# Kernel tuning notes

Hardware: AMD Instinct MI355X
Metric: run time of the kernel (lower is better)

The kernel has to match this reference:

```python
import jax, jax.numpy as jnp
import numpy as np

V, E, H, L, C = 50257, 256, 256, 2, 64
B, T = 4, 48
MASK_ID = 103
EPS = 1e-5
SAMPLE_KEY = jax.random.key(1234)


def lstm_cell(x, h, c, Wih, Whh, bih, bhh):
    # PyTorch gate order: i, f, g, o
    z = x @ Wih.T + h @ Whh.T + (bih + bhh)  # [B,4H]
    i, f, g, o = jnp.split(z, 4, axis=-1)
    c = jax.nn.sigmoid(f) * c + jax.nn.sigmoid(i) * jnp.tanh(g)
    h = jax.nn.sigmoid(o) * jnp.tanh(c)
    return h, c


def setup_inputs() -> dict:
    key = jax.random.key(0)
    ks = jax.random.split(key, 16)
    g = lambda k, s: (jax.random.normal(k, s, dtype=jnp.float32) * 0.05)
    emb = g(ks[0], (V, E)).at[0].set(0.0)  # padding_idx=0 row zeroed
    params = dict(
        emb=emb,
        W_e2e=g(ks[1], (H, E)), b_e2e=jnp.zeros((H,), jnp.float32),
        W_e2d=g(ks[2], (H, E)), b_e2d=jnp.zeros((H,), jnp.float32),
        enc_Wih=g(ks[3], (L, 4 * H, H)), enc_Whh=g(ks[4], (L, 4 * H, H)),
        enc_bih=jnp.zeros((L, 4 * H), jnp.float32), enc_bhh=jnp.zeros((L, 4 * H), jnp.float32),
        dec_Wih=g(ks[5], (L, 4 * H, H)), dec_Whh=g(ks[6], (L, 4 * H, H)),
        dec_bih=jnp.zeros((L, 4 * H), jnp.float32), dec_bhh=jnp.zeros((L, 4 * H), jnp.float32),
        W_cls=g(ks[7], (C, 1)), b_cls=jnp.zeros((C,), jnp.float32),
        W_fc1=g(ks[8], (H + C, H + C)), b_fc1=jnp.zeros((H + C,), jnp.float32),
        ln_g=jnp.ones((H + C,), jnp.float32), ln_b=jnp.zeros((H + C,), jnp.float32),
        W_fc2=g(ks[9], (V, H + C)), b_fc2=jnp.zeros((V,), jnp.float32),
    )
    input_ids = jax.random.randint(ks[10], (B, T), 0, V, dtype=jnp.int32)
    mask_pos = jax.random.bernoulli(ks[11], 0.3, (B, T))  # ensure masked slots exist
    input_ids = jnp.where(mask_pos, jnp.int32(MASK_ID), input_ids)
    attention_mask = jnp.ones((B, T), jnp.int32)
    classification_labels = jax.random.bernoulli(ks[12], 0.5, (B,)).astype(jnp.float32)
    return dict(input_ids=input_ids, attention_mask=attention_mask,
                classification_labels=classification_labels, **params)


def _forward(input_ids, classification_labels, emb, W_e2e, b_e2e, W_e2d, b_e2d,
             enc_Wih, enc_Whh, enc_bih, enc_bhh, dec_Wih, dec_Whh, dec_bih, dec_bhh,
             W_cls, b_cls, W_fc1, b_fc1, ln_g, ln_b, W_fc2, b_fc2):
    f32 = jnp.float32
    # ---- encoder: embed -> linear+relu (dropout=eval identity) -> 2-layer LSTM ----
    xe = jax.nn.relu(emb[input_ids] @ W_e2e.T + b_e2e)  # [B,T,H]
    xs = jnp.swapaxes(xe, 0, 1)  # [T,B,H]
    h0 = jnp.zeros((L, B, H), f32)

    def enc_step(hc, xj):
        h, c = hc
        cur, hs, cs = xj, [], []
        for l in range(L):
            nh, nc = lstm_cell(cur, h[l], c[l], enc_Wih[l], enc_Whh[l], enc_bih[l], enc_bhh[l])
            hs.append(nh); cs.append(nc); cur = nh
        return (jnp.stack(hs), jnp.stack(cs)), None

    (h, c), _ = jax.lax.scan(enc_step, (h0, h0), xs)

    # classifier states are loop-invariant in the original (hoisted, same math)
    cls_states = classification_labels[:, None] @ W_cls.T + b_cls  # [B,C]

    tokens0 = jnp.zeros((B, T), input_ids.dtype).at[:, 0].set(input_ids[:, 0])

    def decode_step(carry, t):
        tokens, h, c = carry
        # re-embed the ENTIRE current prefix, as the original does each step
        x = jax.nn.relu(emb[tokens] @ W_e2d.T + b_e2d)  # [B,T,H]
        xs_t = jnp.swapaxes(x, 0, 1)  # [T,B,H]

        def mstep(hc, inp):
            hh, cc = hc
            xj, j = inp
            cur, hs, cs = xj, [], []
            for l in range(L):
                nh, nc = lstm_cell(cur, hh[l], cc[l], dec_Wih[l], dec_Whh[l], dec_bih[l], dec_bhh[l])
                hs.append(nh); cs.append(nc); cur = nh
            nh, nc = jnp.stack(hs), jnp.stack(cs)
            valid = j < t  # only positions 0..t-1 are real prefix tokens
            hh = jnp.where(valid, nh, hh)
            cc = jnp.where(valid, nc, cc)
            return (hh, cc), hh[-1]

        (h, c), ys = jax.lax.scan(mstep, (h, c), (xs_t, jnp.arange(T)))
        dec_out = jax.lax.dynamic_index_in_dim(ys, t - 1, axis=0, keepdims=False)  # [B,H]

        z = jnp.concatenate([dec_out, cls_states], axis=-1)  # [B,H+C]
        z1 = jax.nn.relu(z @ W_fc1.T + b_fc1)
        mu = z1.mean(-1, keepdims=True)
        var = ((z1 - mu) ** 2).mean(-1, keepdims=True)
        z1 = (z1 - mu) * jax.lax.rsqrt(var + EPS) * ln_g + ln_b
        logits = z1 @ W_fc2.T + b_fc2  # [B,V]
        logp = jax.nn.log_softmax(logits, axis=-1)

        gumb = jax.random.gumbel(jax.random.fold_in(SAMPLE_KEY, t), logp.shape)
        sampled = jnp.argmax(logp + gumb, axis=-1)  # [B] categorical sample
        slp = jnp.take_along_axis(logp, sampled[:, None], axis=-1)[:, 0]  # [B]

        cur_tok = jnp.take(input_ids, t, axis=1)  # [B]
        next_tok = jnp.where(cur_tok == MASK_ID, sampled.astype(tokens.dtype), cur_tok)
        tokens = jax.lax.dynamic_update_slice(tokens, next_tok[:, None], (0, t))
        return (tokens, h, c), slp

    (tokens, h, c), slps = jax.lax.scan(decode_step, (tokens0, h, c), jnp.arange(1, T))
    scores = jnp.concatenate([jnp.zeros((B, 1), f32), slps.T], axis=1)  # [B,T]
    return scores, tokens


def reference(input_ids, attention_mask, classification_labels, emb, W_e2e, b_e2e,
              W_e2d, b_e2d, enc_Wih, enc_Whh, enc_bih, enc_bhh, dec_Wih, dec_Whh,
              dec_bih, dec_bhh, W_cls, b_cls, W_fc1, b_fc1, ln_g, ln_b, W_fc2, b_fc2):
    # attention_mask is accepted but unused, matching the original forward
    return _forward(input_ids, classification_labels, emb, W_e2e, b_e2e, W_e2d, b_e2d,
                    enc_Wih, enc_Whh, enc_bih, enc_bhh, dec_Wih, dec_Whh, dec_bih, dec_bhh,
                    W_cls, b_cls, W_fc1, b_fc1, ln_g, ln_b, W_fc2, b_fc2)
```

## Files before the change

kernel.cpp:

```cpp
#include <hip/hip_runtime.h>
#include <stdint.h>
#include <stddef.h>
#include <math.h>


#define PARTITIONABLE_PRNG 1

namespace s2sr {

constexpr int kV = 50257, kE = 256, kH = 256, kCc = 64, kB = 4, kT = 48;
constexpr int kZ = kH + kCc;
constexpr int kG = 4 * kH;
constexpr int kMask = 103;
constexpr float kEps = 1e-5f;
constexpr float kTiny = 1.17549435e-38f;

constexpr int NWG = 256, TPB = 256;
constexpr int NCL = 32;
constexpr int LEAD = 32;
constexpr int GANG0 = 33;
constexpr int NGANG = NWG - GANG0;
constexpr int RPW = (kV + NGANG - 1) / NGANG;
constexpr int NPX = 16;

constexpr int SH_H0 = 0;
constexpr int SH_H1 = 1024;
constexpr int SH_P0 = 2048;
constexpr int SH_P1 = 3072;
constexpr int SH_Z  = 4096;
constexpr int SH_TOT = 4608;
constexpr int LD_ZIN = 0;
constexpr int LD_Z1  = 1280;
constexpr int LD_CLS = 2560;
constexpr int LD_LSE = 2816;
constexpr int LD_WPS = 2820;

struct alignas(128) Tag { unsigned v; unsigned _p[31]; };
struct alignas(128) GOut {
  unsigned long long key[kB];
  float ps[kB];
  unsigned tag;
  unsigned _p[19];
};

struct SyncBlk {
  Tag ictr, igen;
  Tag ctag[NCL];
  Tag ptok[NPX];
  Tag hzT;
  Tag zT;
  Tag eT;
  GOut gout[NGANG];
};

struct WS {
  SyncBlk s;
  float h0buf[2][kB][kH];
  float h1buf[2][kB][kH];
  float hz[2][kB][kH];
  float z1n[2][kB][kZ];
  float xcur[kB][kH];
  float xd0[kB][kH];
  float px0[kT][kB][kG];
  float pxe[kT][kB][kG];
};

__device__ __forceinline__ float aldf(const float* p) {
  return __hip_atomic_load(p, __ATOMIC_RELAXED, __HIP_MEMORY_SCOPE_AGENT);
}
__device__ __forceinline__ void astf(float* p, float v) {
  __hip_atomic_store(p, v, __ATOMIC_RELAXED, __HIP_MEMORY_SCOPE_AGENT);
}
__device__ __forceinline__ unsigned ldu(const unsigned* p) {
  return __hip_atomic_load(p, __ATOMIC_RELAXED, __HIP_MEMORY_SCOPE_AGENT);
}
__device__ __forceinline__ void relTag(Tag* tg, unsigned v) {
  __hip_atomic_store(&tg->v, v, __ATOMIC_RELEASE, __HIP_MEMORY_SCOPE_AGENT);
}
template <int SLP>
__device__ __forceinline__ void spinTag(Tag* tg, unsigned tgt) {
  if (threadIdx.x == 0) {
    while (ldu(&tg->v) < tgt) __builtin_amdgcn_s_sleep(SLP);
    __atomic_signal_fence(__ATOMIC_ACQUIRE);
  }
  __syncthreads();
}
__device__ __forceinline__ void cbar(SyncBlk* sb, unsigned& ep, int cw) {
  __syncthreads();
  ep += 1u;
  const int tid = (int)threadIdx.x;
  if (tid == 0) relTag(&sb->ctag[cw], ep);
  if (tid < NCL) {
    while (ldu(&sb->ctag[tid].v) < ep) {}
    __atomic_signal_fence(__ATOMIC_ACQUIRE);
  }
  __syncthreads();
}
__device__ __forceinline__ void wait_ptok(SyncBlk* sb, unsigned tgt) {
  if (threadIdx.x < NPX) {
    while (ldu(&sb->ptok[threadIdx.x].v) < tgt) {}
    __atomic_signal_fence(__ATOMIC_ACQUIRE);
  }
  __syncthreads();
}
__device__ __forceinline__ void gbar(SyncBlk* sb, unsigned tgt) {
  __syncthreads();
  if (threadIdx.x == 0) {
    const unsigned old = __hip_atomic_fetch_add(&sb->ictr.v, 1u, __ATOMIC_RELEASE,
                                                __HIP_MEMORY_SCOPE_AGENT);
    if (old == tgt - 1u) relTag(&sb->igen, tgt);
    while (ldu(&sb->igen.v) < tgt) __builtin_amdgcn_s_sleep(2);
    __atomic_signal_fence(__ATOMIC_ACQUIRE);
  }
  __syncthreads();
}

__device__ __forceinline__ unsigned rotl32(unsigned v, int n) {
  return (v << n) | (v >> (32 - n));
}
__device__ __forceinline__ void tf2x32(unsigned k0, unsigned k1, unsigned x0, unsigned x1,
                                       unsigned& o0, unsigned& o1) {
  const unsigned k2 = k0 ^ k1 ^ 0x1BD11BDAu;
  unsigned v0 = x0 + k0, v1 = x1 + k1;
  v0 += v1; v1 = rotl32(v1, 13); v1 ^= v0;
  v0 += v1; v1 = rotl32(v1, 15); v1 ^= v0;
  v0 += v1; v1 = rotl32(v1, 26); v1 ^= v0;
  v0 += v1; v1 = rotl32(v1, 6);  v1 ^= v0;
  v0 += k1; v1 += k2 + 1u;
  v0 += v1; v1 = rotl32(v1, 17); v1 ^= v0;
  v0 += v1; v1 = rotl32(v1, 29); v1 ^= v0;
  v0 += v1; v1 = rotl32(v1, 16); v1 ^= v0;
  v0 += v1; v1 = rotl32(v1, 24); v1 ^= v0;
  v0 += k2; v1 += k0 + 2u;
  v0 += v1; v1 = rotl32(v1, 13); v1 ^= v0;
  v0 += v1; v1 = rotl32(v1, 15); v1 ^= v0;
  v0 += v1; v1 = rotl32(v1, 26); v1 ^= v0;
  v0 += v1; v1 = rotl32(v1, 6);  v1 ^= v0;
  v0 += k0; v1 += k1 + 3u;
  v0 += v1; v1 = rotl32(v1, 17); v1 ^= v0;
  v0 += v1; v1 = rotl32(v1, 29); v1 ^= v0;
  v0 += v1; v1 = rotl32(v1, 16); v1 ^= v0;
  v0 += v1; v1 = rotl32(v1, 24); v1 ^= v0;
  v0 += k1; v1 += k2 + 4u;
  v0 += v1; v1 = rotl32(v1, 13); v1 ^= v0;
  v0 += v1; v1 = rotl32(v1, 15); v1 ^= v0;
  v0 += v1; v1 = rotl32(v1, 26); v1 ^= v0;
  v0 += v1; v1 = rotl32(v1, 6);  v1 ^= v0;
  o0 = v0 + k2; o1 = v1 + k0 + 5u;
}
__device__ __forceinline__ unsigned rbits(unsigned k0, unsigned k1, unsigned i) {
#if PARTITIONABLE_PRNG
  unsigned a, b; tf2x32(k0, k1, 0u, i, a, b);
  return a ^ b;
#else
  constexpr unsigned HALF = (unsigned)((kB * kV + 1) / 2);
  unsigned a, b;
  if (i < HALF) { tf2x32(k0, k1, i, i + HALF, a, b); return a; }
  tf2x32(k0, k1, i - HALF, i, a, b); return b;
#endif
}
__device__ __forceinline__ float gumbel_from_bits(unsigned bits) {
  float f = __uint_as_float((bits >> 9) | 0x3f800000u) - 1.0f;
  f = fmaxf(f, kTiny);
  return -logf(-logf(f));
}
__device__ __forceinline__ unsigned ordkey(float f) {
  const unsigned u = __float_as_uint(f);
  return (u & 0x80000000u) ? ~u : (u | 0x80000000u);
}
__device__ __forceinline__ unsigned long long shflx64(unsigned long long v, int m) {
  unsigned lo = (unsigned)v, hi = (unsigned)(v >> 32);
  lo = (unsigned)__shfl_xor((int)lo, m, 64);
  hi = (unsigned)__shfl_xor((int)hi, m, 64);
  return ((unsigned long long)hi << 32) | (unsigned long long)lo;
}
__device__ __forceinline__ float sigm(float x) { return 1.0f / (1.0f + expf(-x)); }

template <bool STREAM>
__device__ __forceinline__ void lstm_tick(
    SyncBlk* sb, WS* ws, float* shf, int cw, unsigned& ep, int cc,
    bool do_l0, bool do_l1, const float* px,
    const float* pW0, const float* pW1,
    const float4* w0r, const float4* w1r,
    float biasr, float& c0, float& c1, int grow, int r, int w, int hzt) {
  const int tid = (int)threadIdx.x;
  float pxv0 = 0.f, pxv1 = 0.f, pxv2 = 0.f, pxv3 = 0.f;
  if (do_l0 && tid < 32) {
    pxv0 = aldf(px + 0 * kG + grow);
    pxv1 = aldf(px + 1 * kG + grow);
    pxv2 = aldf(px + 2 * kG + grow);
    pxv3 = aldf(px + 3 * kG + grow);
  }
  {
    const float* h0p = &ws->h0buf[(cc + 1) & 1][0][0];
#pragma unroll
    for (int i = 0; i < 4; ++i) shf[SH_H0 + tid + i * 256] = aldf(h0p + tid + i * 256);
    if (do_l1) {
      const float* h1p = &ws->h1buf[cc & 1][0][0];
#pragma unroll
      for (int i = 0; i < 4; ++i) shf[SH_H1 + tid + i * 256] = aldf(h1p + tid + i * 256);
    }
  }
  __syncthreads();
  float4 wv0[8], wv1[16];
  if (do_l0) {
#pragma unroll
    for (int i = 0; i < 8; ++i)
      wv0[i] = STREAM ? *reinterpret_cast<const float4*>(pW0 + i * 4) : w0r[i];
  }
  if (do_l1) {
#pragma unroll
    for (int i = 0; i < 16; ++i)
      wv1[i] = STREAM ? *reinterpret_cast<const float4*>(pW1 + i * 4) : w1r[i];
  }
  if (do_l0) {
    const float* A = &shf[SH_H0 + w * 32];
    float a0 = 0.f, a1 = 0.f, a2 = 0.f, a3 = 0.f;
#pragma unroll
    for (int i = 0; i < 8; ++i) {
      const float4 wv = wv0[i];
      const float4 x0 = *reinterpret_cast<const float4*>(A + 0 * 256 + i * 4);
      const float4 x1 = *reinterpret_cast<const float4*>(A + 1 * 256 + i * 4);
      const float4 x2 = *reinterpret_cast<const float4*>(A + 2 * 256 + i * 4);
      const float4 x3 = *reinterpret_cast<const float4*>(A + 3 * 256 + i * 4);
      a0 = fmaf(wv.x, x0.x, a0); a0 = fmaf(wv.y, x0.y, a0); a0 = fmaf(wv.z, x0.z, a0); a0 = fmaf(wv.w, x0.w, a0);
      a1 = fmaf(wv.x, x1.x, a1); a1 = fmaf(wv.y, x1.y, a1); a1 = fmaf(wv.z, x1.z, a1); a1 = fmaf(wv.w, x1.w, a1);
      a2 = fmaf(wv.x, x2.x, a2); a2 = fmaf(wv.y, x2.y, a2); a2 = fmaf(wv.z, x2.z, a2); a2 = fmaf(wv.w, x2.w, a2);
      a3 = fmaf(wv.x, x3.x, a3); a3 = fmaf(wv.y, x3.y, a3); a3 = fmaf(wv.z, x3.z, a3); a3 = fmaf(wv.w, x3.w, a3);
    }
    *reinterpret_cast<float4*>(&shf[SH_P0 + w * 128 + r * 4]) = float4{a0, a1, a2, a3};
  }
  if (do_l1) {
    const float* Bp = (w < 4) ? &shf[SH_H0 + w * 64] : &shf[SH_H1 + (w - 4) * 64];
    float a0 = 0.f, a1 = 0.f, a2 = 0.f, a3 = 0.f;
#pragma unroll
    for (int i = 0; i < 16; ++i) {
      const float4 wv = wv1[i];
      const float4 x0 = *reinterpret_cast<const float4*>(Bp + 0 * 256 + i * 4);
      const float4 x1 = *reinterpret_cast<const float4*>(Bp + 1 * 256 + i * 4);
      const float4 x2 = *reinterpret_cast<const float4*>(Bp + 2 * 256 + i * 4);
      const float4 x3 = *reinterpret_cast<const float4*>(Bp + 3 * 256 + i * 4);
      a0 = fmaf(wv.x, x0.x, a0); a0 = fmaf(wv.y, x0.y, a0); a0 = fmaf(wv.z, x0.z, a0); a0 = fmaf(wv.w, x0.w, a0);
      a1 = fmaf(wv.x, x1.x, a1); a1 = fmaf(wv.y, x1.y, a1); a1 = fmaf(wv.z, x1.z, a1); a1 = fmaf(wv.w, x1.w, a1);
      a2 = fmaf(wv.x, x2.x, a2); a2 = fmaf(wv.y, x2.y, a2); a2 = fmaf(wv.z, x2.z, a2); a2 = fmaf(wv.w, x2.w, a2);
      a3 = fmaf(wv.x, x3.x, a3); a3 = fmaf(wv.y, x3.y, a3); a3 = fmaf(wv.z, x3.z, a3); a3 = fmaf(wv.w, x3.w, a3);
    }
    *reinterpret_cast<float4*>(&shf[SH_P1 + w * 128 + r * 4]) = float4{a0, a1, a2, a3};
  }
  __syncthreads();
  if (tid < 64) {
    const int L = tid >> 5, rr = tid & 31;
    const bool en = L ? do_l1 : do_l0;
    if (en) {
      const int base = (L ? SH_P1 : SH_P0) + rr * 4;
      float4 z = float4{0.f, 0.f, 0.f, 0.f};
#pragma unroll
      for (int w2 = 0; w2 < 8; ++w2) {
        const float4 p = *reinterpret_cast<const float4*>(&shf[base + w2 * 128]);
        z.x += p.x; z.y += p.y; z.z += p.z; z.w += p.w;
      }
      z.x += biasr; z.y += biasr; z.z += biasr; z.w += biasr;
      if (L == 0) { z.x += pxv0; z.y += pxv1; z.z += pxv2; z.w += pxv3; }
      *reinterpret_cast<float4*>(&shf[SH_Z + L * 128 + rr * 4]) = z;
    }
  }
  __syncthreads();
  if (tid < 64) {
    const int L = tid >> 5, slot = tid & 31;
    const bool en = L ? do_l1 : do_l0;
    if (en) {
      const int b = slot >> 3, u = slot & 7;
      const int zb = SH_Z + L * 128 + u * 16 + b;
      const float zi = shf[zb], zf = shf[zb + 4], zg = shf[zb + 8], zo = shf[zb + 12];
      const float cs = L ? c1 : c0;
      const float cn = sigm(zf) * cs + sigm(zi) * tanhf(zg);
      const float hn = sigm(zo) * tanhf(cn);
      if (L) {
        c1 = cn;
        astf(&ws->h1buf[(cc + 1) & 1][b][cw * 8 + u], hn);
        if (hzt >= 0) astf(&ws->hz[hzt & 1][b][cw * 8 + u], hn);
      } else {
        c0 = cn;
        astf(&ws->h0buf[cc & 1][b][cw * 8 + u], hn);
      }
    }
  }
  cbar(sb, ep, cw);
}

__global__ void __launch_bounds__(TPB, 1) s2s_kernel(
    const int* __restrict__ input_ids, const float* __restrict__ labels,
    const float* __restrict__ emb,
    const float* __restrict__ W_e2e, const float* __restrict__ b_e2e,
    const float* __restrict__ W_e2d, const float* __restrict__ b_e2d,
    const float* __restrict__ encWih, const float* __restrict__ encWhh,
    const float* __restrict__ encbih, const float* __restrict__ encbhh,
    const float* __restrict__ decWih, const float* __restrict__ decWhh,
    const float* __restrict__ decbih, const float* __restrict__ decbhh,
    const float* __restrict__ W_cls, const float* __restrict__ b_cls,
    const float* __restrict__ Wfc1, const float* __restrict__ bfc1,
    const float* __restrict__ lng, const float* __restrict__ lnb,
    const float* __restrict__ W_fc2, const float* __restrict__ b_fc2,
    float* __restrict__ out, WS* __restrict__ ws) {
  const int wg = (int)blockIdx.x;
  const int tid = (int)threadIdx.x;
  SyncBlk* sb = &ws->s;
  __shared__ __align__(16) float shf[SH_TOT];
  __shared__ unsigned long long shk[16];
  __shared__ int shi[8];

  if (wg < kB * kT) {
    const int b = wg / kT, j = wg % kT;
    const int id = input_ids[b * kT + j];
    for (int i = tid; i < kE; i += 256) shf[i] = emb[(size_t)id * kE + i];
    __syncthreads();
    const float* wr = W_e2e + (size_t)tid * kE;
    float acc = b_e2e[tid];
    for (int k = 0; k < kE; k += 4) {
      const float4 wv = *reinterpret_cast<const float4*>(wr + k);
      const float4 xv = *reinterpret_cast<const float4*>(&shf[k]);
      acc = fmaf(xv.x, wv.x, acc); acc = fmaf(xv.y, wv.y, acc);
      acc = fmaf(xv.z, wv.z, acc); acc = fmaf(xv.w, wv.w, acc);
    }
    __syncthreads();
    shf[256 + tid] = fmaxf(acc, 0.f);
  } else if (wg == 192) {
    if (tid < kB) {
      const int t0 = input_ids[tid * kT];
      out[tid * kT] = 0.f;
      out[kB * kT + tid * kT] = (float)t0;
    }
  } else if (wg == 193) {
    const float* wr = W_e2d + (size_t)tid * kE;
    const float* e0 = emb + (size_t)input_ids[0 * kT] * kE;
    const float* e1 = emb + (size_t)input_ids[1 * kT] * kE;
    const float* e2 = emb + (size_t)input_ids[2 * kT] * kE;
    const float* e3 = emb + (size_t)input_ids[3 * kT] * kE;
    const float bb = b_e2d[tid];
    float a0 = bb, a1 = bb, a2 = bb, a3 = bb;
    for (int k = 0; k < kE; k += 4) {
      const float4 wv = *reinterpret_cast<const float4*>(wr + k);
      const float4 v0 = *reinterpret_cast<const float4*>(e0 + k);
      const float4 v1 = *reinterpret_cast<const float4*>(e1 + k);
      const float4 v2 = *reinterpret_cast<const float4*>(e2 + k);
      const float4 v3 = *reinterpret_cast<const float4*>(e3 + k);
      a0 = fmaf(v0.x, wv.x, a0); a0 = fmaf(v0.y, wv.y, a0); a0 = fmaf(v0.z, wv.z, a0); a0 = fmaf(v0.w, wv.w, a0);
      a1 = fmaf(v1.x, wv.x, a1); a1 = fmaf(v1.y, wv.y, a1); a1 = fmaf(v1.z, wv.z, a1); a1 = fmaf(v1.w, wv.w, a1);
      a2 = fmaf(v2.x, wv.x, a2); a2 = fmaf(v2.y, wv.y, a2); a2 = fmaf(v2.z, wv.z, a2); a2 = fmaf(v2.w, wv.w, a2);
      a3 = fmaf(v3.x, wv.x, a3); a3 = fmaf(v3.y, wv.y, a3); a3 = fmaf(v3.z, wv.z, a3); a3 = fmaf(v3.w, wv.w, a3);
    }
    astf(&ws->xd0[0][tid], fmaxf(a0, 0.f));
    astf(&ws->xd0[1][tid], fmaxf(a1, 0.f));
    astf(&ws->xd0[2][tid], fmaxf(a2, 0.f));
    astf(&ws->xd0[3][tid], fmaxf(a3, 0.f));
  }
  gbar(sb, (unsigned)NWG);

  if (wg < kB * kT) {
    const int b = wg / kT, j = wg % kT;
#pragma unroll
    for (int rr = 0; rr < 4; ++rr) {
      const int g = rr * 256 + tid;
      const float* wr = encWih + (size_t)g * kH;
      float acc = 0.f;
      for (int k = 0; k < kH; k += 4) {
        const float4 wv = *reinterpret_cast<const float4*>(wr + k);
        const float4 xv = *reinterpret_cast<const float4*>(&shf[256 + k]);
        acc = fmaf(xv.x, wv.x, acc); acc = fmaf(xv.y, wv.y, acc);
        acc = fmaf(xv.z, wv.z, acc); acc = fmaf(xv.w, wv.w, acc);
      }
      astf(&ws->pxe[j][0][0] + (size_t)b * kG + g, acc);
    }
  } else if (wg >= 192 && wg < 208) {
    const int w2 = wg - 192, b = w2 >> 2, q = w2 & 3;
    const int g = q * 256 + tid;
    for (int i = tid; i < kH; i += 256) shf[i] = aldf(&ws->xd0[b][i]);
    __syncthreads();
    const float* wr = decWih + (size_t)g * kH;
    float acc = 0.f;
    for (int k = 0; k < kH; k += 4) {
      const float4 wv = *reinterpret_cast<const float4*>(wr + k);
      const float4 xv = *reinterpret_cast<const float4*>(&shf[k]);
      acc = fmaf(xv.x, wv.x, acc); acc = fmaf(xv.y, wv.y, acc);
      acc = fmaf(xv.z, wv.z, acc); acc = fmaf(xv.w, wv.w, acc);
    }
    astf(&ws->px0[0][0][0] + (size_t)b * kG + g, acc);
  }
  gbar(sb, (unsigned)(2 * NWG));

  if (wg < NCL) {
    const int cw = wg;
    const int r = tid & 31, w = tid >> 5;
    const int grow = (r & 3) * 256 + cw * 8 + (r >> 2);
    const int L = tid >> 5;
    unsigned ep = 0;
    float c0 = 0.f, c1 = 0.f;
    float biasr = 0.f;
    if (tid < 64)
      biasr = (L == 0) ? encbih[grow] + encbhh[grow]
                       : encbih[kG + grow] + encbhh[kG + grow];
    const float* pW0e = encWhh + (size_t)grow * kH + w * 32;
    const float* pW1e = (w < 4)
        ? encWih + (size_t)kG * kH + (size_t)grow * kH + w * 64
        : encWhh + (size_t)kG * kH + (size_t)grow * kH + (w - 4) * 64;
    int cc = 0;
    for (int j = 0; j < kT; ++j, ++cc)
      lstm_tick<true>(sb, ws, shf, cw, ep, cc, true, j > 0, &ws->pxe[j][0][0],
                      pW0e, pW1e, nullptr, nullptr, biasr, c0, c1, grow, r, w, -1);
    lstm_tick<true>(sb, ws, shf, cw, ep, cc, false, true, nullptr,
                    pW0e, pW1e, nullptr, nullptr, biasr, c0, c1, grow, r, w, -1);
    float4 w0d[8], w1d[16];
    {
      const float* p0 = decWhh + (size_t)grow * kH + w * 32;
#pragma unroll
      for (int i = 0; i < 8; ++i) w0d[i] = *reinterpret_cast<const float4*>(p0 + i * 4);
      const float* p1 = (w < 4)
          ? decWih + (size_t)kG * kH + (size_t)grow * kH + w * 64
          : decWhh + (size_t)kG * kH + (size_t)grow * kH + (w - 4) * 64;
#pragma unroll
      for (int i = 0; i < 16; ++i) w1d[i] = *reinterpret_cast<const float4*>(p1 + i * 4);
      if (tid < 64)
        biasr = (L == 0) ? decbih[grow] + decbhh[grow]
                         : decbih[kG + grow] + decbhh[kG + grow];
    }
    for (int t = 1; t < kT; ++t) {
      for (int j = 0; j < t; ++j, ++cc) {
        const bool d1 = (j > 0) || (t >= 2);
        const int hzt = (j == 0 && t >= 2) ? (t - 1) : -1;
        if (j == t - 1 && t >= 2) wait_ptok(sb, (unsigned)(t - 1));
        lstm_tick<false>(sb, ws, shf, cw, ep, cc, true, d1, &ws->px0[j][0][0],
                         nullptr, nullptr, w0d, w1d, biasr, c0, c1, grow, r, w, hzt);
        if (hzt >= 0 && cw == 0 && tid == 0) relTag(&sb->hzT, (unsigned)hzt);
      }
    }
    lstm_tick<false>(sb, ws, shf, cw, ep, cc, false, true, nullptr,
                     nullptr, nullptr, w0d, w1d, biasr, c0, c1, grow, r, w, kT - 1);
    if (cw == 0 && tid == 0) relTag(&sb->hzT, (unsigned)(kT - 1));
  } else if (wg == LEAD) {
    if (tid < kB * kCc) {
      const int b = tid >> 6, c = tid & 63;
      shf[LD_CLS + tid] = fmaf(labels[b], W_cls[c], b_cls[c]);
    }
    __syncthreads();
    for (int t = 1; t < kT; ++t) {
      spinTag<1>(&sb->hzT, (unsigned)t);
      for (int i = tid; i < kB * kZ; i += 256) {
        const int b = i / kZ, k = i - b * kZ;
        shf[LD_ZIN + i] = (k < kH) ? aldf(&ws->hz[t & 1][b][k])
                                   : shf[LD_CLS + b * kCc + (k - kH)];
      }
      __syncthreads();
#pragma unroll
      for (int rep = 0; rep < 5; ++rep) {
        const int task = tid + rep * 256;
        const int b = task / kZ, o = task - b * kZ;
        const float* wr = Wfc1 + (size_t)o * kZ;
        const float* zz = &shf[LD_ZIN + b * kZ];
        float acc = bfc1[o];
        for (int k = 0; k < kZ; k += 4) {
          const float4 wv = *reinterpret_cast<const float4*>(wr + k);
          const float4 zv = *reinterpret_cast<const float4*>(zz + k);
          acc = fmaf(zv.x, wv.x, acc); acc = fmaf(zv.y, wv.y, acc);
          acc = fmaf(zv.z, wv.z, acc); acc = fmaf(zv.w, wv.w, acc);
        }
        shf[LD_Z1 + task] = fmaxf(acc, 0.f);
      }
      __syncthreads();
      {
        const int b = tid >> 6, ln = tid & 63;
        float s1 = 0.f, s2 = 0.f;
        for (int i = ln; i < kZ; i += 64) {
          const float v = shf[LD_Z1 + b * kZ + i]; s1 += v; s2 += v * v;
        }
#pragma unroll
        for (int o = 32; o > 0; o >>= 1) { s1 += __shfl_xor(s1, o, 64); s2 += __shfl_xor(s2, o, 64); }
        const float mu = s1 * (1.0f / kZ);
        const float var = s2 * (1.0f / kZ) - mu * mu;
        const float rs = 1.0f / sqrtf(var + kEps);
        for (int i = ln; i < kZ; i += 64) {
          const float v = fmaf((shf[LD_Z1 + b * kZ + i] - mu) * rs, lng[i], lnb[i]);
          shf[LD_Z1 + b * kZ + i] = v;
          astf(&ws->z1n[t & 1][b][i], v);
        }
      }
      __syncthreads();
      if (tid == 0) relTag(&sb->zT, (unsigned)t);
      if (tid < NGANG) {
        while (ldu(&sb->gout[tid].tag) < (unsigned)t) __builtin_amdgcn_s_sleep(2);
        __atomic_signal_fence(__ATOMIC_ACQUIRE);
      }
      __syncthreads();
      {
        unsigned long long kk[kB];
        float pp[kB];
        if (tid < NGANG) {
          const GOut* g = &sb->gout[tid];
#pragma unroll
          for (int b = 0; b < kB; ++b) {
            kk[b] = __hip_atomic_load(&g->key[b], __ATOMIC_RELAXED, __HIP_MEMORY_SCOPE_AGENT);
            pp[b] = aldf(&g->ps[b]);
          }
        } else {
#pragma unroll
          for (int b = 0; b < kB; ++b) { kk[b] = 0ull; pp[b] = 0.f; }
        }
#pragma unroll
        for (int b = 0; b < kB; ++b) {
#pragma unroll
          for (int m = 1; m < 64; m <<= 1) {
            const unsigned long long ko = shflx64(kk[b], m);
            pp[b] += __shfl_xor(pp[b], m, 64);
            if (ko > kk[b]) kk[b] = ko;
          }
        }
        if ((tid & 63) == 0) {
          const int wv = tid >> 6;
#pragma unroll
          for (int b = 0; b < kB; ++b) { shk[wv * kB + b] = kk[b]; shf[LD_WPS + wv * kB + b] = pp[b]; }
        }
      }
      __syncthreads();
      if (tid < kB) {
        const int b = tid;
        unsigned long long key = shk[b];
        float s = shf[LD_WPS + b];
        for (int wv = 1; wv < 4; ++wv) {
          const unsigned long long ko = shk[wv * kB + b];
          if (ko > key) key = ko;
          s += shf[LD_WPS + wv * kB + b];
        }
        const int samp = (int)(0xFFFFFFFFu - (unsigned)(key & 0xFFFFFFFFull));
        const float lse = logf(s);
        const int cur = input_ids[b * kT + t];
        const int nxt = (cur == kMask) ? samp : cur;
        out[kB * kT + b * kT + t] = (float)nxt;
        shi[b] = nxt; shi[4 + b] = samp;
        shf[LD_LSE + b] = lse;
      }
      __syncthreads();
      if (t < kT - 1) {
        const float* wr = W_e2d + (size_t)tid * kE;
        const float* e0 = emb + (size_t)shi[0] * kE;
        const float* e1 = emb + (size_t)shi[1] * kE;
        const float* e2 = emb + (size_t)shi[2] * kE;
        const float* e3 = emb + (size_t)shi[3] * kE;
        const float bb = b_e2d[tid];
        float a0 = bb, a1 = bb, a2 = bb, a3 = bb;
        for (int k = 0; k < kE; k += 4) {
          const float4 wv = *reinterpret_cast<const float4*>(wr + k);
          const float4 v0 = *reinterpret_cast<const float4*>(e0 + k);
          const float4 v1 = *reinterpret_cast<const float4*>(e1 + k);
          const float4 v2 = *reinterpret_cast<const float4*>(e2 + k);
          const float4 v3 = *reinterpret_cast<const float4*>(e3 + k);
          a0 = fmaf(v0.x, wv.x, a0); a0 = fmaf(v0.y, wv.y, a0); a0 = fmaf(v0.z, wv.z, a0); a0 = fmaf(v0.w, wv.w, a0);
          a1 = fmaf(v1.x, wv.x, a1); a1 = fmaf(v1.y, wv.y, a1); a1 = fmaf(v1.z, wv.z, a1); a1 = fmaf(v1.w, wv.w, a1);
          a2 = fmaf(v2.x, wv.x, a2); a2 = fmaf(v2.y, wv.y, a2); a2 = fmaf(v2.z, wv.z, a2); a2 = fmaf(v2.w, wv.w, a2);
          a3 = fmaf(v3.x, wv.x, a3); a3 = fmaf(v3.y, wv.y, a3); a3 = fmaf(v3.z, wv.z, a3); a3 = fmaf(v3.w, wv.w, a3);
        }
        astf(&ws->xcur[0][tid], fmaxf(a0, 0.f));
        astf(&ws->xcur[1][tid], fmaxf(a1, 0.f));
        astf(&ws->xcur[2][tid], fmaxf(a2, 0.f));
        astf(&ws->xcur[3][tid], fmaxf(a3, 0.f));
        __syncthreads();
        if (tid == 0) relTag(&sb->eT, (unsigned)t);
      }
      {
        const int b = tid >> 6, lane = tid & 63;
        const int sp = shi[4 + b];
        const float* wr = W_fc2 + (size_t)sp * kZ;
        float acc = 0.f;
#pragma unroll
        for (int i = 0; i < 5; ++i)
          acc = fmaf(shf[LD_Z1 + b * kZ + lane + i * 64], wr[lane + i * 64], acc);
#pragma unroll
        for (int o = 32; o > 0; o >>= 1) acc += __shfl_xor(acc, o, 64);
        if (lane == 0) out[b * kT + t] = acc + b_fc2[sp] - shf[LD_LSE + b];
      }
      __syncthreads();
    }
  } else {
    const int gi = wg - GANG0;
    const int start = gi * RPW;
    const int cnt = (RPW < kV - start) ? RPW : (kV - start);
    const bool act = tid < cnt;
    const int row = start + tid;
    for (int t = 1; t < kT; ++t) {
      spinTag<16>(&sb->zT, (unsigned)t);
      for (int i = tid; i < kB * kZ; i += 256) shf[i] = aldf(&ws->z1n[t & 1][0][0] + i);
      __syncthreads();
      unsigned fk0, fk1;
      tf2x32(0u, 1234u, 0u, (unsigned)t, fk0, fk1);
      float lv[kB] = {0.f, 0.f, 0.f, 0.f};
      if (act) {
        const float* wr = W_fc2 + (size_t)row * kZ;
        const float bb = b_fc2[row];
        float a0 = bb, a1 = bb, a2 = bb, a3 = bb;
        for (int k = 0; k < kZ; k += 4) {
          const float4 wv = *reinterpret_cast<const float4*>(wr + k);
          const float4 z0 = *reinterpret_cast<const float4*>(&shf[0 * kZ + k]);
          const float4 z1 = *reinterpret_cast<const float4*>(&shf[1 * kZ + k]);
          const float4 z2 = *reinterpret_cast<const float4*>(&shf[2 * kZ + k]);
          const float4 z3 = *reinterpret_cast<const float4*>(&shf[3 * kZ + k]);
          a0 = fmaf(z0.x, wv.x, a0); a0 = fmaf(z0.y, wv.y, a0); a0 = fmaf(z0.z, wv.z, a0); a0 = fmaf(z0.w, wv.w, a0);
          a1 = fmaf(z1.x, wv.x, a1); a1 = fmaf(z1.y, wv.y, a1); a1 = fmaf(z1.z, wv.z, a1); a1 = fmaf(z1.w, wv.w, a1);
          a2 = fmaf(z2.x, wv.x, a2); a2 = fmaf(z2.y, wv.y, a2); a2 = fmaf(z2.z, wv.z, a2); a2 = fmaf(z2.w, wv.w, a2);
          a3 = fmaf(z3.x, wv.x, a3); a3 = fmaf(z3.y, wv.y, a3); a3 = fmaf(z3.z, wv.z, a3); a3 = fmaf(z3.w, wv.w, a3);
        }
        lv[0] = a0; lv[1] = a1; lv[2] = a2; lv[3] = a3;
      }
#pragma unroll
      for (int b = 0; b < kB; ++b) {
        unsigned long long key = 0ull;
        float sv = 0.f;
        if (act) {
          const unsigned bits = rbits(fk0, fk1, (unsigned)(b * kV + row));
          const float pv = lv[b] + gumbel_from_bits(bits);
          key = ((unsigned long long)ordkey(pv) << 32) |
                (unsigned long long)(0xFFFFFFFFu - (unsigned)row);
          sv = expf(lv[b]);
        }
#pragma unroll
        for (int m = 1; m < 64; m <<= 1) {
          const unsigned long long ko = shflx64(key, m);
          sv += __shfl_xor(sv, m, 64);
          if (ko > key) key = ko;
        }
        if ((tid & 63) == 0) { shk[(tid >> 6) * kB + b] = key; shf[1408 + (tid >> 6) * kB + b] = sv; }
      }
      __syncthreads();
      if (tid == 0) {
        GOut* g = &sb->gout[gi];
#pragma unroll
        for (int b = 0; b < kB; ++b) {
          unsigned long long key = shk[b];
          float s = shf[1408 + b];
          for (int w2 = 1; w2 < 4; ++w2) {
            const unsigned long long ko = shk[w2 * kB + b];
            if (ko > key) key = ko;
            s += shf[1408 + w2 * kB + b];
          }
          __hip_atomic_store(&g->key[b], key, __ATOMIC_RELAXED, __HIP_MEMORY_SCOPE_AGENT);
          astf(&g->ps[b], s);
        }
        __hip_atomic_store(&g->tag, (unsigned)t, __ATOMIC_RELEASE, __HIP_MEMORY_SCOPE_AGENT);
      }
      if (gi < NPX && t < kT - 1) {
        spinTag<4>(&sb->eT, (unsigned)t);
        for (int i = tid; i < kB * kH; i += 256) shf[i] = aldf(&ws->xcur[0][0] + i);
        __syncthreads();
        {
          const int rowg = gi * 64 + (tid & 63), b = tid >> 6;
          const float* wr = decWih + (size_t)rowg * kH;
          const float* xz = &shf[b * kH];
          float acc = 0.f;
          for (int k = 0; k < kH; k += 4) {
            const float4 wv = *reinterpret_cast<const float4*>(wr + k);
            const float4 xv = *reinterpret_cast<const float4*>(xz + k);
            acc = fmaf(xv.x, wv.x, acc); acc = fmaf(xv.y, wv.y, acc);
            acc = fmaf(xv.z, wv.z, acc); acc = fmaf(xv.w, wv.w, acc);
          }
          astf(&ws->px0[t][0][0] + (size_t)b * kG + rowg, acc);
        }
        __syncthreads();
        if (tid == 0) relTag(&sb->ptok[gi], (unsigned)t);
      }
      __syncthreads();
    }
  }
}

}

extern "C" void kernel_launch(void* const* d_in, const int* in_sizes, int n_in,
                              void* d_out, int out_size, void* d_ws, size_t ws_size,
                              hipStream_t stream) {
  using namespace s2sr;
  (void)in_sizes; (void)n_in; (void)out_size;
  if (ws_size < sizeof(WS)) return;
  const int*   input_ids = (const int*)d_in[0];
  const float* labels    = (const float*)d_in[2];
  const float* emb       = (const float*)d_in[3];
  const float* W_e2e     = (const float*)d_in[4];
  const float* b_e2e     = (const float*)d_in[5];
  const float* W_e2d     = (const float*)d_in[6];
  const float* b_e2d     = (const float*)d_in[7];
  const float* encWih    = (const float*)d_in[8];
  const float* encWhh    = (const float*)d_in[9];
  const float* encbih    = (const float*)d_in[10];
  const float* encbhh    = (const float*)d_in[11];
  const float* decWih    = (const float*)d_in[12];
  const float* decWhh    = (const float*)d_in[13];
  const float* decbih    = (const float*)d_in[14];
  const float* decbhh    = (const float*)d_in[15];
  const float* W_cls     = (const float*)d_in[16];
  const float* b_cls     = (const float*)d_in[17];
  const float* W_fc1     = (const float*)d_in[18];
  const float* b_fc1     = (const float*)d_in[19];
  const float* ln_g      = (const float*)d_in[20];
  const float* ln_b      = (const float*)d_in[21];
  const float* W_fc2     = (const float*)d_in[22];
  const float* b_fc2     = (const float*)d_in[23];

  hipMemsetAsync(d_ws, 0, (size_t)offsetof(WS, hz), stream);
  hipLaunchKernelGGL(s2s_kernel, dim3(NWG), dim3(TPB), 0, stream,
      input_ids, labels, emb, W_e2e, b_e2e, W_e2d, b_e2d,
      encWih, encWhh, encbih, encbhh, decWih, decWhh, decbih, decbhh,
      W_cls, b_cls, W_fc1, b_fc1, ln_g, ln_b, W_fc2, b_fc2,
      (float*)d_out, (WS*)d_ws);
}
```

Measured before the change: 8.574 ms.

## Replace cluster barrier with epoch-tagged hidden-state words and per-wave tags

The recurrent LSTM workgroups no longer meet at a cluster-wide barrier after every tick. Each hidden value is now published as a 64-bit word that packs the float with its tick index. Readers spin on the individual words until they carry the expected epoch, so data and flag arrive in a single store. The single-flag handoffs (hzT, zT, eT, ptok) become per-workgroup or per-wave tags, which removes several __syncthreads before signalling. The cost is doubled hidden-state traffic and more spin loads, plus a larger memset region.

Result: faster. 7.600 ms (-11.4%).

```diff
diff --git a/kernel.cpp b/kernel.cpp
--- a/kernel.cpp
+++ b/kernel.cpp
@@ -45,19 +45,17 @@
 
 struct SyncBlk {
   Tag ictr, igen;
-  Tag ctag[NCL];
-  Tag ptok[NPX];
-  Tag hzT;
-  Tag zT;
-  Tag eT;
+  Tag ptok4[NPX][4];
+  Tag ztag4[4];
+  Tag etok4[4];
+  Tag hztag[NCL];
   GOut gout[NGANG];
 };
 
 struct WS {
   SyncBlk s;
-  float h0buf[2][kB][kH];
-  float h1buf[2][kB][kH];
-  float hz[2][kB][kH];
+  unsigned long long hc[2][2][NCL][32];
+  float hzbuf[2][kB][kH];
   float z1n[2][kB][kZ];
   float xcur[kB][kH];
   float xd0[kB][kH];
@@ -74,34 +72,14 @@
 __device__ __forceinline__ unsigned ldu(const unsigned* p) {
   return __hip_atomic_load(p, __ATOMIC_RELAXED, __HIP_MEMORY_SCOPE_AGENT);
 }
+__device__ __forceinline__ unsigned long long ld64(const unsigned long long* p) {
+  return __hip_atomic_load(p, __ATOMIC_RELAXED, __HIP_MEMORY_SCOPE_AGENT);
+}
+__device__ __forceinline__ void st64(unsigned long long* p, unsigned long long v) {
+  __hip_atomic_store(p, v, __ATOMIC_RELAXED, __HIP_MEMORY_SCOPE_AGENT);
+}
 __device__ __forceinline__ void relTag(Tag* tg, unsigned v) {
   __hip_atomic_store(&tg->v, v, __ATOMIC_RELEASE, __HIP_MEMORY_SCOPE_AGENT);
-}
-template <int SLP>
-__device__ __forceinline__ void spinTag(Tag* tg, unsigned tgt) {
-  if (threadIdx.x == 0) {
-    while (ldu(&tg->v) < tgt) __builtin_amdgcn_s_sleep(SLP);
-    __atomic_signal_fence(__ATOMIC_ACQUIRE);
-  }
-  __syncthreads();
-}
-__device__ __forceinline__ void cbar(SyncBlk* sb, unsigned& ep, int cw) {
-  __syncthreads();
-  ep += 1u;
-  const int tid = (int)threadIdx.x;
-  if (tid == 0) relTag(&sb->ctag[cw], ep);
-  if (tid < NCL) {
-    while (ldu(&sb->ctag[tid].v) < ep) {}
-    __atomic_signal_fence(__ATOMIC_ACQUIRE);
-  }
-  __syncthreads();
-}
-__device__ __forceinline__ void wait_ptok(SyncBlk* sb, unsigned tgt) {
-  if (threadIdx.x < NPX) {
-    while (ldu(&sb->ptok[threadIdx.x].v) < tgt) {}
-    __atomic_signal_fence(__ATOMIC_ACQUIRE);
-  }
-  __syncthreads();
 }
 __device__ __forceinline__ void gbar(SyncBlk* sb, unsigned tgt) {
   __syncthreads();
@@ -178,11 +156,11 @@
 
 template <bool STREAM>
 __device__ __forceinline__ void lstm_tick(
-    SyncBlk* sb, WS* ws, float* shf, int cw, unsigned& ep, int cc,
-    bool do_l0, bool do_l1, const float* px,
-    const float* pW0, const float* pW1,
-    const float4* w0r, const float4* w1r,
-    float biasr, float& c0, float& c1, int grow, int r, int w, int hzt) {
+    WS* ws, float* shf, int cw, int cc, bool do_l0, bool do_l1,
+    const float* px, const float* pW0, const float* pW1,
+    const float4* w0r, const float4* w1r, float biasr,
+    float& c0, float& c1, float& h0last, float& h1last,
+    int grow, int r, int w, int hzt) {
   const int tid = (int)threadIdx.x;
   float pxv0 = 0.f, pxv1 = 0.f, pxv2 = 0.f, pxv3 = 0.f;
   if (do_l0 && tid < 32) {
@@ -192,13 +170,28 @@
     pxv3 = aldf(px + 3 * kG + grow);
   }
   {
-    const float* h0p = &ws->h0buf[(cc + 1) & 1][0][0];
-#pragma unroll
-    for (int i = 0; i < 4; ++i) shf[SH_H0 + tid + i * 256] = aldf(h0p + tid + i * 256);
-    if (do_l1) {
-      const float* h1p = &ws->h1buf[cc & 1][0][0];
-#pragma unroll
-      for (int i = 0; i < 4; ++i) shf[SH_H1 + tid + i * 256] = aldf(h1p + tid + i * 256);
+    const unsigned long long* base = &ws->hc[(cc + 1) & 1][0][0][0];
+    const unsigned exp = (unsigned)cc;
+    unsigned long long v[8];
+#pragma unroll
+    for (int k = 0; k < 8; ++k) v[k] = ld64(base + tid * 8 + k);
+    unsigned pend = 0;
+#pragma unroll
+    for (int k = 0; k < 8; ++k) if ((unsigned)v[k] != exp) pend |= 1u << k;
+    while (pend) {
+#pragma unroll
+      for (int k = 0; k < 8; ++k)
+        if (pend & (1u << k)) v[k] = ld64(base + tid * 8 + k);
+#pragma unroll
+      for (int k = 0; k < 8; ++k)
+        if ((unsigned)v[k] == exp) pend &= ~(1u << k);
+    }
+#pragma unroll
+    for (int k = 0; k < 8; ++k) {
+      const int c = tid * 8 + k, L = c >> 10, rem = c & 1023;
+      const int wg2 = rem >> 5, s = rem & 31;
+      shf[L * 1024 + (s >> 3) * 256 + wg2 * 8 + (s & 7)] =
+          __uint_as_float((unsigned)(v[k] >> 32));
     }
   }
   __syncthreads();
@@ -266,26 +259,25 @@
   }
   __syncthreads();
   if (tid < 64) {
-    const int L = tid >> 5, slot = tid & 31;
+    const int L = tid >> 5, slot = tid & 31, b = slot >> 3, u = slot & 7;
     const bool en = L ? do_l1 : do_l0;
+    float hn;
     if (en) {
-      const int b = slot >> 3, u = slot & 7;
       const int zb = SH_Z + L * 128 + u * 16 + b;
       const float zi = shf[zb], zf = shf[zb + 4], zg = shf[zb + 8], zo = shf[zb + 12];
       const float cs = L ? c1 : c0;
       const float cn = sigm(zf) * cs + sigm(zi) * tanhf(zg);
-      const float hn = sigm(zo) * tanhf(cn);
-      if (L) {
-        c1 = cn;
-        astf(&ws->h1buf[(cc + 1) & 1][b][cw * 8 + u], hn);
-        if (hzt >= 0) astf(&ws->hz[hzt & 1][b][cw * 8 + u], hn);
-      } else {
-        c0 = cn;
-        astf(&ws->h0buf[cc & 1][b][cw * 8 + u], hn);
-      }
-    }
-  }
-  cbar(sb, ep, cw);
+      hn = sigm(zo) * tanhf(cn);
+      if (L) c1 = cn; else c0 = cn;
+    } else {
+      hn = L ? h1last : h0last;
+    }
+    if (L) h1last = hn; else h0last = hn;
+    st64(&ws->hc[cc & 1][L][cw][slot],
+         ((unsigned long long)__float_as_uint(hn) << 32) |
+         (unsigned long long)(unsigned)(cc + 1));
+    if (L && hzt >= 0) astf(&ws->hzbuf[hzt & 1][b][cw * 8 + u], hn);
+  }
 }
 
 __global__ void __launch_bounds__(TPB, 1) s2s_kernel(
@@ -393,8 +385,7 @@
     const int r = tid & 31, w = tid >> 5;
     const int grow = (r & 3) * 256 + cw * 8 + (r >> 2);
     const int L = tid >> 5;
-    unsigned ep = 0;
-    float c0 = 0.f, c1 = 0.f;
+    float c0 = 0.f, c1 = 0.f, h0last = 0.f, h1last = 0.f;
     float biasr = 0.f;
     if (tid < 64)
       biasr = (L == 0) ? encbih[grow] + encbhh[grow]
@@ -405,10 +396,13 @@
         : encWhh + (size_t)kG * kH + (size_t)grow * kH + (w - 4) * 64;
     int cc = 0;
     for (int j = 0; j < kT; ++j, ++cc)
-      lstm_tick<true>(sb, ws, shf, cw, ep, cc, true, j > 0, &ws->pxe[j][0][0],
-                      pW0e, pW1e, nullptr, nullptr, biasr, c0, c1, grow, r, w, -1);
-    lstm_tick<true>(sb, ws, shf, cw, ep, cc, false, true, nullptr,
-                    pW0e, pW1e, nullptr, nullptr, biasr, c0, c1, grow, r, w, -1);
+      lstm_tick<true>(ws, shf, cw, cc, true, j > 0, &ws->pxe[j][0][0],
+                      pW0e, pW1e, nullptr, nullptr, biasr, c0, c1,
+                      h0last, h1last, grow, r, w, -1);
+    lstm_tick<true>(ws, shf, cw, cc, false, true, nullptr,
+                    pW0e, pW1e, nullptr, nullptr, biasr, c0, c1,
+                    h0last, h1last, grow, r, w, -1);
+    ++cc;
     float4 w0d[8], w1d[16];
     {
       const float* p0 = decWhh + (size_t)grow * kH + w * 32;
@@ -427,15 +421,24 @@
       for (int j = 0; j < t; ++j, ++cc) {
         const bool d1 = (j > 0) || (t >= 2);
         const int hzt = (j == 0 && t >= 2) ? (t - 1) : -1;
-        if (j == t - 1 && t >= 2) wait_ptok(sb, (unsigned)(t - 1));
-        lstm_tick<false>(sb, ws, shf, cw, ep, cc, true, d1, &ws->px0[j][0][0],
-                         nullptr, nullptr, w0d, w1d, biasr, c0, c1, grow, r, w, hzt);
-        if (hzt >= 0 && cw == 0 && tid == 0) relTag(&sb->hzT, (unsigned)hzt);
-      }
-    }
-    lstm_tick<false>(sb, ws, shf, cw, ep, cc, false, true, nullptr,
-                     nullptr, nullptr, w0d, w1d, biasr, c0, c1, grow, r, w, kT - 1);
-    if (cw == 0 && tid == 0) relTag(&sb->hzT, (unsigned)(kT - 1));
+        if (j == t - 1 && t >= 2) {
+          if (tid < 64) {
+            Tag* p = &sb->ptok4[tid >> 2][tid & 3];
+            while (ldu(&p->v) < (unsigned)(t - 1)) {}
+            __atomic_signal_fence(__ATOMIC_ACQUIRE);
+          }
+          __syncthreads();
+        }
+        lstm_tick<false>(ws, shf, cw, cc, true, d1, &ws->px0[j][0][0],
+                         nullptr, nullptr, w0d, w1d, biasr, c0, c1,
+                         h0last, h1last, grow, r, w, hzt);
+        if (hzt >= 0 && tid == 0) relTag(&sb->hztag[cw], (unsigned)hzt);
+      }
+    }
+    lstm_tick<false>(ws, shf, cw, cc, false, true, nullptr,
+                     nullptr, nullptr, w0d, w1d, biasr, c0, c1,
+                     h0last, h1last, grow, r, w, kT - 1);
+    if (tid == 0) relTag(&sb->hztag[cw], (unsigned)(kT - 1));
   } else if (wg == LEAD) {
     if (tid < kB * kCc) {
       const int b = tid >> 6, c = tid & 63;
@@ -443,10 +446,14 @@
     }
     __syncthreads();
     for (int t = 1; t < kT; ++t) {
-      spinTag<1>(&sb->hzT, (unsigned)t);
+      if (tid < NCL) {
+        while (ldu(&sb->hztag[tid].v) < (unsigned)t) __builtin_amdgcn_s_sleep(1);
+        __atomic_signal_fence(__ATOMIC_ACQUIRE);
+      }
+      __syncthreads();
       for (int i = tid; i < kB * kZ; i += 256) {
         const int b = i / kZ, k = i - b * kZ;
-        shf[LD_ZIN + i] = (k < kH) ? aldf(&ws->hz[t & 1][b][k])
+        shf[LD_ZIN + i] = (k < kH) ? aldf(&ws->hzbuf[t & 1][b][k])
                                    : shf[LD_CLS + b * kCc + (k - kH)];
       }
       __syncthreads();
@@ -482,9 +489,8 @@
           shf[LD_Z1 + b * kZ + i] = v;
           astf(&ws->z1n[t & 1][b][i], v);
         }
-      }
-      __syncthreads();
-      if (tid == 0) relTag(&sb->zT, (unsigned)t);
+        if (ln == 0) relTag(&sb->ztag4[b], (unsigned)t);
+      }
       if (tid < NGANG) {
         while (ldu(&sb->gout[tid].tag) < (unsigned)t) __builtin_amdgcn_s_sleep(2);
         __atomic_signal_fence(__ATOMIC_ACQUIRE);
@@ -496,10 +502,7 @@
         if (tid < NGANG) {
           const GOut* g = &sb->gout[tid];
 #pragma unroll
-          for (int b = 0; b < kB; ++b) {
-            kk[b] = __hip_atomic_load(&g->key[b], __ATOMIC_RELAXED, __HIP_MEMORY_SCOPE_AGENT);
-            pp[b] = aldf(&g->ps[b]);
-          }
+          for (int b = 0; b < kB; ++b) { kk[b] = ld64(&g->key[b]); pp[b] = aldf(&g->ps[b]); }
         } else {
 #pragma unroll
           for (int b = 0; b < kB; ++b) { kk[b] = 0ull; pp[b] = 0.f; }
@@ -561,8 +564,7 @@
         astf(&ws->xcur[1][tid], fmaxf(a1, 0.f));
         astf(&ws->xcur[2][tid], fmaxf(a2, 0.f));
         astf(&ws->xcur[3][tid], fmaxf(a3, 0.f));
-        __syncthreads();
-        if (tid == 0) relTag(&sb->eT, (unsigned)t);
+        if ((tid & 63) == 0) relTag(&sb->etok4[tid >> 6], (unsigned)t);
       }
       {
         const int b = tid >> 6, lane = tid & 63;
@@ -585,7 +587,11 @@
     const bool act = tid < cnt;
     const int row = start + tid;
     for (int t = 1; t < kT; ++t) {
-      spinTag<16>(&sb->zT, (unsigned)t);
+      if (tid < 4) {
+        while (ldu(&sb->ztag4[tid].v) < (unsigned)t) __builtin_amdgcn_s_sleep(16);
+        __atomic_signal_fence(__ATOMIC_ACQUIRE);
+      }
+      __syncthreads();
       for (int i = tid; i < kB * kZ; i += 256) shf[i] = aldf(&ws->z1n[t & 1][0][0] + i);
       __syncthreads();
       unsigned fk0, fk1;
@@ -639,13 +645,18 @@
             if (ko > key) key = ko;
             s += shf[1408 + w2 * kB + b];
           }
-          __hip_atomic_store(&g->key[b], key, __ATOMIC_RELAXED, __HIP_MEMORY_SCOPE_AGENT);
+          st64(&g->key[b], key);
           astf(&g->ps[b], s);
         }
         __hip_atomic_store(&g->tag, (unsigned)t, __ATOMIC_RELEASE, __HIP_MEMORY_SCOPE_AGENT);
       }
+      __syncthreads();
       if (gi < NPX && t < kT - 1) {
-        spinTag<4>(&sb->eT, (unsigned)t);
+        if (tid < 4) {
+          while (ldu(&sb->etok4[tid].v) < (unsigned)t) __builtin_amdgcn_s_sleep(8);
+          __atomic_signal_fence(__ATOMIC_ACQUIRE);
+        }
+        __syncthreads();
         for (int i = tid; i < kB * kH; i += 256) shf[i] = aldf(&ws->xcur[0][0] + i);
         __syncthreads();
         {
@@ -660,9 +671,8 @@
             acc = fmaf(xv.z, wv.z, acc); acc = fmaf(xv.w, wv.w, acc);
           }
           astf(&ws->px0[t][0][0] + (size_t)b * kG + rowg, acc);
-        }
-        __syncthreads();
-        if (tid == 0) relTag(&sb->ptok[gi], (unsigned)t);
+          if ((tid & 63) == 0) relTag(&sb->ptok4[gi][tid >> 6], (unsigned)t);
+        }
       }
       __syncthreads();
     }
@@ -701,7 +711,7 @@
   const float* W_fc2     = (const float*)d_in[22];
   const float* b_fc2     = (const float*)d_in[23];
 
-  hipMemsetAsync(d_ws, 0, (size_t)offsetof(WS, hz), stream);
+  hipMemsetAsync(d_ws, 0, (size_t)offsetof(WS, xd0), stream);
   hipLaunchKernelGGL(s2s_kernel, dim3(NWG), dim3(TPB), 0, stream,
       input_ids, labels, emb, W_e2e, b_e2e, W_e2d, b_e2d,
       encWih, encWhh, encbih, encbhh, decWih, decWhh, decbih, decbhh,
```
